# Optimization experiments

Hardware: AMD Instinct MI355X
Metric: run time of the kernel (lower is better)

## Reference

```python
import jax, jax.numpy as jnp
import numpy as np

B, N, K = 4, 8192, 10
_DIMS = [(12, 64), (64, 64), (128, 64), (64, 64), (128, 64), (192, 1024), (1216, 256), (256, 256), (256, 128), (128, 2)]


def setup_inputs() -> dict:
    key = jax.random.key(0)
    keys = jax.random.split(key, 12)
    inp = {"targets": jax.random.normal(keys[0], (B, N, 3), dtype=jnp.float32)}
    for i, (ci, co) in enumerate(_DIMS):
        a = float(np.sqrt(0.75 / ci))  # init_params: uniform(-sqrt(0.75/fan_in), +)
        inp[f"w{i + 1}"] = jax.random.uniform(keys[i + 1], (ci, co), minval=-a, maxval=a, dtype=jnp.float32)
    inp["prelu_a"] = 0.25 * jnp.ones((10,), jnp.float32)  # nn.PReLU default slope
    return inp


def _prelu(x, a):
    return jnp.where(x >= 0, x, a * x)


def _graph_features(x, k):
    # x: [N, C] -> edge features [N, k, 2C] (knn gather, diff, concat center)
    x2 = jnp.sum(x * x, axis=-1)
    d = x2[:, None] + x2[None, :] - 2.0 * (x @ x.T)  # [N, N] sq dists
    _, idx = jax.lax.top_k(-d, k)  # k nearest (includes self)
    nb = x[idx]  # [N, k, C]
    xr = jnp.broadcast_to(x[:, None, :], nb.shape)
    return jnp.concatenate([nb - xr, xr], axis=-1)


def _edge_conv(x, wa_list, k):
    # x: [B, N, C]; shared-MLP on edge features then max over k neighbors
    f = jax.vmap(lambda xb: _graph_features(xb, k))(x)  # [B, N, k, 2C]
    for w, a in wa_list:
        f = _prelu(f @ w, a)
    return jnp.max(f, axis=-2)  # [B, N, Cout]


def _forward(targets, ws, pa):
    # loss_f(targets) = 0.5*||targets||^2  =>  targets_grad = targets
    g = jax.grad(lambda t: 0.5 * jnp.sum(t * t))(targets)
    x = jnp.concatenate([targets, g], axis=-1)  # [B, N, 6]; hidden_features=0
    x1 = _edge_conv(x, [(ws[0], pa[0]), (ws[1], pa[1])], K)
    x2 = _edge_conv(x1, [(ws[2], pa[2]), (ws[3], pa[3])], K)
    x3 = _edge_conv(x2, [(ws[4], pa[4])], K)
    x4 = jnp.concatenate([x1, x2, x3], axis=-1)  # [B, N, 192]
    x5 = _prelu(x4 @ ws[5], pa[5])  # [B, N, 1024]
    x5 = jnp.broadcast_to(jnp.max(x5, axis=-2, keepdims=True), x5.shape)  # global max, repeated
    y = jnp.concatenate([x1, x2, x3, x5], axis=-1)  # [B, N, 1216]
    for i in range(6, 10):  # dropout is identity at eval
        y = _prelu(y @ ws[i], pa[i])
    return y[..., : 2]  # lr = y[..., :num_losses*2]; hidden slice is empty


def reference(targets, w1, w2, w3, w4, w5, w6, w7, w8, w9, w10, prelu_a):
    ws = [w1, w2, w3, w4, w5, w6, w7, w8, w9, w10]
    return _forward(targets, ws, prelu_a)
```

## Files before the change

kernel.cpp:

```cpp
#include <hip/hip_runtime.h>
#include <math.h>

#define NPTS 8192
#define KNNK 10

typedef __attribute__((ext_vector_type(8))) short bf16x8s;
typedef __attribute__((ext_vector_type(4))) float f32x4;

__device__ __forceinline__ float preluf(float v, float a){ return v >= 0.f ? v : a*v; }
__device__ __forceinline__ float4 f4fma(float a, float4 b, float4 c){
  return make_float4(fmaf(a,b.x,c.x), fmaf(a,b.y,c.y), fmaf(a,b.z,c.z), fmaf(a,b.w,c.w));
}

__device__ __forceinline__ void gl_lds16(const void* g, void* l){
  __builtin_amdgcn_global_load_lds((const __attribute__((address_space(1))) void*)g,
                                   (__attribute__((address_space(3))) void*)l, 16, 0, 0);
}
__device__ __forceinline__ void gl_lds4(const void* g, void* l){
  __builtin_amdgcn_global_load_lds((const __attribute__((address_space(1))) void*)g,
                                   (__attribute__((address_space(3))) void*)l, 4, 0, 0);
}

__device__ __forceinline__ void kinsd2(double* bk, float& g9, float pbd9, float d, int j){
  if (__any(d < g9)) {
    double t = (double)d;
    t = __longlong_as_double(__double_as_longlong(t) | (unsigned long long)(unsigned)j);
    #pragma unroll
    for (int s=0;s<10;++s){
      double mn = fmin(bk[s], t);
      double mx = fmax(bk[s], t);
      bk[s] = mn; t = mx;
    }
    g9 = fminf((float)bk[9], pbd9);
  }
}

__device__ __forceinline__ unsigned bfsplit2(float a, float b, unsigned& lo2){
  unsigned ua = __float_as_uint(a), ub = __float_as_uint(b);
  unsigned ha = (ua + 0x7FFFu + ((ua>>16)&1u)) & 0xFFFF0000u;
  unsigned hb = (ub + 0x7FFFu + ((ub>>16)&1u)) & 0xFFFF0000u;
  float ra = a - __uint_as_float(ha);
  float rb = b - __uint_as_float(hb);
  unsigned la = __float_as_uint(ra), lb = __float_as_uint(rb);
  unsigned qa = (la + 0x7FFFu + ((la>>16)&1u)) >> 16;
  unsigned qb = (lb + 0x7FFFu + ((lb>>16)&1u)) & 0xFFFF0000u;
  lo2 = qa | qb;
  return (ha >> 16) | hb;
}

__global__ __launch_bounds__(256) void prep0_kernel(const float* __restrict__ T,
                                                    float* __restrict__ x0,
                                                    float* __restrict__ sqn){
  int p = blockIdx.x*256 + threadIdx.x;
  float t0 = T[p*3+0], t1 = T[p*3+1], t2 = T[p*3+2];
  *(float4*)(x0 + (size_t)p*4) = make_float4(t0,t1,t2,0.f);
  float s = fmaf(t0,t0,0.f); s = fmaf(t1,t1,s); s = fmaf(t2,t2,s); s = fmaf(0.f,0.f,s);
  sqn[p] = s;
}

__global__ __launch_bounds__(256, 3) void knn64_kernel(const unsigned short* __restrict__ Xh,
                                                       const unsigned short* __restrict__ Xl,
                                                       const float* __restrict__ sqn,
                                                       double* __restrict__ pk){
  __shared__ __align__(16) unsigned char smem[52224];
  float* sx2j = (float*)(smem + 51200);
  double* lst = (double*)smem;

  const int b   = blockIdx.y;
  const int q0  = blockIdx.x * 128;
  const int jh  = blockIdx.z;
  const int NT  = (jh == 2) ? 22 : 21;
  const int jbase = jh * 2688;
  const int tid = threadIdx.x;
  const int L   = tid & 63;
  const int w   = tid >> 6;
  const int lm  = L & 15;
  const int kg  = L >> 4;
  const int rl  = L & 31;
  const int th  = L >> 5;

  float* dchw = (float*)(smem + 32768 + w*4608);

  const size_t bbase = (size_t)b * NPTS;

  bf16x8s ah[2][2], al[2][2];
  {
    const char* Ahp = (const char*)Xh + (bbase + q0 + w*32 + lm)*128;
    const char* Alp = (const char*)Xl + (bbase + q0 + w*32 + lm)*128;
    #pragma unroll
    for (int mt=0;mt<2;++mt)
      #pragma unroll
      for (int kc=0;kc<2;++kc){
        ah[mt][kc] = *(const bf16x8s*)(Ahp + mt*2048 + kc*64 + kg*16);
        al[mt][kc] = *(const bf16x8s*)(Alp + mt*2048 + kc*64 + kg*16);
      }
  }
  float x2qr[2][4];
  #pragma unroll
  for (int mt=0;mt<2;++mt)
    #pragma unroll
    for (int r=0;r<4;++r)
      x2qr[mt][r] = sqn[bbase + q0 + w*32 + mt*16 + kg*4 + r];

  const int srow = L >> 3;
  const unsigned soff = (unsigned)(((L & 7) ^ srow) << 4);
  const char* srch = (const char*)Xh + (bbase + (size_t)jbase + w*32 + srow)*128 + soff;
  const char* srcl = (const char*)Xl + (bbase + (size_t)jbase + w*32 + srow)*128 + soff;
  const float* sx2jsrc = sqn + bbase + jbase + w*64 + L;

  #pragma unroll
  for (int i=0;i<4;++i){
    gl_lds16(srch + i*1024, smem + w*4096 + i*1024);
    gl_lds16(srcl + i*1024, smem + 16384 + w*4096 + i*1024);
  }
  if (w < 2) gl_lds4(sx2jsrc, (char*)sx2j + w*256);

  double bk[10];
  float g9 = INFINITY, pbd9 = INFINITY;
  #pragma unroll
  for (int u=0;u<10;++u) bk[u] = (double)INFINITY;

  const char* xjh_c = (const char*)smem;
  const char* xjl_c = (const char*)smem + 16384;
  const unsigned swz = (unsigned)((lm & 7) << 4);

  for (int t = 0; t < NT; ++t) {
    __syncthreads();

    f32x4 acc[2][8];
    #pragma unroll
    for (int mt=0;mt<2;++mt)
      #pragma unroll
      for (int nt=0;nt<8;++nt) acc[mt][nt] = (f32x4){0.f,0.f,0.f,0.f};

    #pragma unroll
    for (int kc=0;kc<2;++kc){
      const unsigned koff = (unsigned)(kc*64 + kg*16) ^ swz;
      #pragma unroll
      for (int nt=0;nt<8;++nt){
        const int rb = (nt*16 + lm)*128;
        bf16x8s bh = *(const bf16x8s*)(xjh_c + rb + koff);
        bf16x8s bl = *(const bf16x8s*)(xjl_c + rb + koff);
        #pragma unroll
        for (int mt=0;mt<2;++mt){
          acc[mt][nt] = __builtin_amdgcn_mfma_f32_16x16x32_bf16(ah[mt][kc], bh, acc[mt][nt], 0,0,0);
          acc[mt][nt] = __builtin_amdgcn_mfma_f32_16x16x32_bf16(ah[mt][kc], bl, acc[mt][nt], 0,0,0);
          acc[mt][nt] = __builtin_amdgcn_mfma_f32_16x16x32_bf16(al[mt][kc], bh, acc[mt][nt], 0,0,0);
        }
      }
    }
    __syncthreads();

    if (t < NT-1){
      const char* nh = srch + (size_t)(t+1)*16384;
      const char* nl = srcl + (size_t)(t+1)*16384;
      #pragma unroll
      for (int i=0;i<4;++i){
        gl_lds16(nh + i*1024, smem + w*4096 + i*1024);
        gl_lds16(nl + i*1024, smem + 16384 + w*4096 + i*1024);
      }
      if (w < 2) gl_lds4(sx2jsrc + (size_t)(t+1)*128, (char*)sx2j + ((t+1)&1)*512 + w*256);
    }

    const int j0 = jbase + t*128;
    const float* x2jb = sx2j + (t&1)*128;

    #pragma unroll
    for (int cb=0; cb<4; ++cb){
      #pragma unroll
      for (int q2=0;q2<2;++q2){
        const int nt = cb*2 + q2;
        const int colc = q2*16 + lm;
        const float xj2 = x2jb[cb*32 + colc];
        #pragma unroll
        for (int mt=0;mt<2;++mt){
          f32x4 c = acc[mt][nt];
          #pragma unroll
          for (int r=0;r<4;++r)
            dchw[(mt*16 + kg*4 + r)*36 + colc] = x2qr[mt][r] + xj2 - 2.0f*c[r];
        }
      }
      asm volatile("" ::: "memory");
      const int jb0 = j0 + cb*32 + th*16;
      #pragma unroll
      for (int c4=0;c4<4;++c4){
        float4 dv = *(const float4*)&dchw[rl*36 + th*16 + c4*4];
        float m4 = fminf(fminf(dv.x,dv.y), fminf(dv.z,dv.w));
        if (__any(m4 < g9)){
          const int jj = jb0 + c4*4;
          kinsd2(bk, g9, pbd9, dv.x, jj);
          kinsd2(bk, g9, pbd9, dv.y, jj+1);
          kinsd2(bk, g9, pbd9, dv.z, jj+2);
          kinsd2(bk, g9, pbd9, dv.w, jj+3);
        }
      }
      asm volatile("" ::: "memory");
      float d9o = (float)bk[9];
      float p9  = __shfl_xor(d9o, 32);
      pbd9 = p9;
      g9 = fminf(d9o, p9);
    }
  }

  __syncthreads();
  #pragma unroll
  for (int u=0;u<10;++u) lst[(w*32 + rl)*20 + th*10 + u] = bk[u];
  __syncthreads();
  if (tid < 128) {
    const double* row = &lst[tid*20];
    int ia=0, ib=0;
    size_t base = ((size_t)jh*(4*NPTS) + bbase + q0 + tid)*10;
    #pragma unroll
    for (int u=0;u<10;++u){
      double ka = row[ia], kb2 = row[10+ib];
      bool ta = ka < kb2;
      pk[base+u] = ta ? ka : kb2;
      ia += ta ? 1 : 0; ib += ta ? 0 : 1;
    }
  }
}

__global__ __launch_bounds__(256, 2) void knn4_kernel(const float* __restrict__ X,
                                                      const float* __restrict__ sqn,
                                                      double* __restrict__ pk){
  __shared__ __align__(16) float xqT[4*132];
  __shared__ __align__(16) float uni[10752];
  __shared__ float s_x2q[128];
  __shared__ float s_x2j[128];
  __shared__ float sbd[2][128];

  const int b   = blockIdx.y;
  const int q0  = blockIdx.x * 128;
  const int jh  = blockIdx.z;
  const int tid = threadIdx.x;
  const int tn  = tid & 15;
  const int tm  = tid >> 4;
  const int tq  = tid & 127;
  const int th  = tid >> 7;

  const float* Xb = X + (size_t)b * NPTS * 4;

  for (int i = tid; i < 128; i += 256) {
    float4 v = *(const float4*)(Xb + (size_t)(q0+i)*4);
    xqT[0*132+i] = v.x; xqT[1*132+i] = v.y; xqT[2*132+i] = v.z; xqT[3*132+i] = v.w;
  }
  if (tid < 128) s_x2q[tid] = sqn[b*NPTS + q0 + tid];

  const int sw  = ((tn>>2)&3) << 2;
  const int bp0 = (tn*8)     ^ sw;
  const int bp1 = (tn*8 + 4) ^ sw;

  double bk[10];
  float g9 = INFINITY, pbd9 = INFINITY;
  #pragma unroll
  for (int u=0;u<10;++u) bk[u] = (double)INFINITY;

  for (int t = 0; t < 32; ++t) {
    const int j0 = jh*4096 + t*128;
    for (int i = tid; i < 128; i += 256) {
      float4 v = *(const float4*)(Xb + (size_t)(j0+i)*4);
      int pj = i ^ (((i>>5)&3) << 2);
      uni[0*132+pj] = v.x; uni[1*132+pj] = v.y; uni[2*132+pj] = v.z; uni[3*132+pj] = v.w;
    }
    if (tid < 128) s_x2j[tid] = sqn[b*NPTS + j0 + tid];
    __syncthreads();

    float acc[8][8];
    #pragma unroll
    for (int i=0;i<8;++i)
      #pragma unroll
      for (int j=0;j<8;++j) acc[i][j] = 0.f;

    #pragma unroll
    for (int kk=0; kk<4; ++kk) {
      float av[8], bv[8];
      *(float4*)&av[0] = *(const float4*)&xqT[kk*132 + tm*8];
      *(float4*)&av[4] = *(const float4*)&xqT[kk*132 + tm*8 + 4];
      *(float4*)&bv[0] = *(const float4*)&uni[kk*132 + bp0];
      *(float4*)&bv[4] = *(const float4*)&uni[kk*132 + bp1];
      #pragma unroll
      for (int i=0;i<8;++i)
        #pragma unroll
        for (int j=0;j<8;++j)
          acc[i][j] = fmaf(av[i], bv[j], acc[i][j]);
    }
    __syncthreads();

    #pragma unroll
    for (int h=0; h<2; ++h) {
      if ((tn>>3) == h) {
        #pragma unroll
        for (int qi=0; qi<8; ++qi) {
          const int row = tm*8 + qi;
          const float xq2 = s_x2q[row];
          float vv[8];
          #pragma unroll
          for (int u=0;u<8;++u)
            vv[u] = xq2 + s_x2j[tn*8 + u] - 2.f*acc[qi][u];
          *(float4*)&uni[row*68 + (tn&7)*8]     = make_float4(vv[0],vv[1],vv[2],vv[3]);
          *(float4*)&uni[row*68 + (tn&7)*8 + 4] = make_float4(vv[4],vv[5],vv[6],vv[7]);
        }
      }
      __syncthreads();
      {
        const int jb0 = j0 + h*64 + th*32;
        #pragma unroll
        for (int c4=0;c4<8;++c4){
          float4 dv = *(const float4*)&uni[tq*68 + th*32 + c4*4];
          int jj = jb0 + c4*4;
          kinsd2(bk, g9, pbd9, dv.x, jj);
          kinsd2(bk, g9, pbd9, dv.y, jj+1);
          kinsd2(bk, g9, pbd9, dv.z, jj+2);
          kinsd2(bk, g9, pbd9, dv.w, jj+3);
        }
      }
      if (h == 1) sbd[th][tq] = (float)bk[9];
      __syncthreads();
      if (h == 1){
        pbd9 = sbd[1^th][tq];
        g9 = fminf((float)bk[9], pbd9);
      }
    }
  }

  double* lst = (double*)uni;
  #pragma unroll
  for (int u=0;u<10;++u) lst[tq*20 + th*10 + u] = bk[u];
  __syncthreads();
  if (tid < 128) {
    const double* row = &lst[tid*20];
    int ia=0, ib=0;
    size_t base = ((size_t)jh*(4*NPTS) + (size_t)b*NPTS + q0 + tid)*10;
    #pragma unroll
    for (int u=0;u<10;++u){
      double ka = row[ia], kb2 = row[10+ib];
      bool ta = ka < kb2;
      pk[base+u] = ta ? ka : kb2;
      ia += ta ? 1 : 0; ib += ta ? 0 : 1;
    }
  }
}

__global__ __launch_bounds__(256) void knnmerge_kernel(const double* __restrict__ pk,
                                                       int* __restrict__ idxout){
  int p = blockIdx.x*256 + threadIdx.x;
  const double* A = pk + (size_t)p*10;
  const double* B = pk + (size_t)(4*NPTS)*10 + (size_t)p*10;
  int ia=0, ib=0;
  int* op = idxout + (size_t)p*10;
  #pragma unroll
  for (int u=0;u<10;++u){
    double ka = A[ia], kb = B[ib];
    bool t = ka < kb;
    op[u] = (int)(__double_as_longlong(t ? ka : kb) & 8191LL);
    ia += t ? 1 : 0; ib += t ? 0 : 1;
  }
}

__global__ __launch_bounds__(256) void knnmerge3_kernel(const double* __restrict__ pk,
                                                        int* __restrict__ idxout){
  int p = blockIdx.x*256 + threadIdx.x;
  const double* A = pk + (size_t)p*10;
  const double* B = pk + (size_t)(4*NPTS)*10 + (size_t)p*10;
  const double* C = pk + (size_t)(8*NPTS)*10 + (size_t)p*10;
  int ia=0, ib=0, ic=0;
  int* op = idxout + (size_t)p*10;
  #pragma unroll
  for (int u=0;u<10;++u){
    double ka = A[ia], kb = B[ib], kc = C[ic];
    bool tab = ka < kb; double mab = tab ? ka : kb;
    bool tc  = mab < kc; double m  = tc ? mab : kc;
    op[u] = (int)(__double_as_longlong(m) & 8191LL);
    ia += (tc && tab)  ? 1 : 0;
    ib += (tc && !tab) ? 1 : 0;
    ic += tc ? 0 : 1;
  }
}

__global__ __launch_bounds__(256) void prepUD64_kernel(const float* __restrict__ XC, int cin,
                                                       const float* __restrict__ W,
                                                       float* __restrict__ U,
                                                       float* __restrict__ D){
  const int tid = threadIdx.x;
  const int w = tid >> 6, o = tid & 63;
  const int p = blockIdx.x*4 + w;
  const float* xr = XC + (size_t)p*192 + cin;
  float zu = 0.f, zd = 0.f;
  #pragma unroll
  for (int c=0;c<64;++c){
    float xc = xr[c];
    float wt = W[c*64 + o];
    float wb = W[(64+c)*64 + o];
    zu = fmaf(xc, wt, zu);
    zd = fmaf(xc, wb - wt, zd);
  }
  U[(size_t)p*64 + o] = zu;
  D[(size_t)p*64 + o] = zd;
}

__global__ __launch_bounds__(256) void prepUD12_kernel(const float* __restrict__ T,
                                                       const float* __restrict__ W1,
                                                       float* __restrict__ U,
                                                       float* __restrict__ D){
  int p = blockIdx.x*256 + threadIdx.x;
  float t[3] = {T[p*3+0], T[p*3+1], T[p*3+2]};
  const float4* W = (const float4*)W1;
  float4 u[16], q[16];
  #pragma unroll
  for (int o=0;o<16;++o){ u[o]=make_float4(0,0,0,0); q[o]=make_float4(0,0,0,0); }
  #pragma unroll
  for (int c=0;c<3;++c){
    const float tc = t[c];
    #pragma unroll
    for (int o=0;o<16;++o){
      float4 ws  = W[c*16+o],     ws2 = W[(c+3)*16+o];
      float4 wq  = W[(c+6)*16+o], wq2 = W[(c+9)*16+o];
      u[o] = f4fma(tc, make_float4(ws.x+ws2.x, ws.y+ws2.y, ws.z+ws2.z, ws.w+ws2.w), u[o]);
      q[o] = f4fma(tc, make_float4(wq.x+wq2.x, wq.y+wq2.y, wq.z+wq2.z, wq.w+wq2.w), q[o]);
    }
  }
  float4* up = (float4*)(U + (size_t)p*64);
  float4* dp = (float4*)(D + (size_t)p*64);
  #pragma unroll
  for (int o=0;o<16;++o){
    up[o] = u[o];
    dp[o] = make_float4(q[o].x-u[o].x, q[o].y-u[o].y, q[o].z-u[o].z, q[o].w-u[o].w);
  }
}

__global__ __launch_bounds__(256) void edge2w_kernel(const float* __restrict__ U,
                                                     const float* __restrict__ Dp,
                                                     const int* __restrict__ idx,
                                                     const float* __restrict__ Wb,
                                                     const float* __restrict__ PA, int paa, int pab,
                                                     float* __restrict__ out, int coff,
                                                     float* __restrict__ sqnout,
                                                     unsigned short* __restrict__ Xh,
                                                     unsigned short* __restrict__ Xl){
  __shared__ __align__(16) float sh[4][10][68];
  const int tid = threadIdx.x;
  const int w = tid >> 6, o = tid & 63;
  const int p = blockIdx.x*4 + w, b = p >> 13;
  const float aa = PA[paa], ab = PA[pab];

  float wreg[64];
  #pragma unroll
  for (int c=0;c<64;++c) wreg[c] = Wb[c*64 + o];

  const float dc = Dp[(size_t)p*64 + o];

  #pragma unroll
  for (int k=0;k<10;++k){
    int nb = idx[p*10 + k];
    float u = U[((size_t)(b<<13)+nb)*64 + o];
    sh[w][k][o] = preluf(u + dc, aa);
  }
  __syncthreads();

  float mx = -INFINITY;
  #pragma unroll 2
  for (int k=0;k<10;++k){
    float a0=0.f,a1=0.f,a2=0.f,a3=0.f;
    #pragma unroll
    for (int c4=0;c4<16;++c4){
      float4 hv = *(const float4*)&sh[w][k][c4*4];
      a0 = fmaf(hv.x, wreg[c4*4+0], a0);
      a1 = fmaf(hv.y, wreg[c4*4+1], a1);
      a2 = fmaf(hv.z, wreg[c4*4+2], a2);
      a3 = fmaf(hv.w, wreg[c4*4+3], a3);
    }
    float z = (a0+a1)+(a2+a3);
    mx = fmaxf(mx, preluf(z, ab));
  }
  out[(size_t)p*192 + coff + o] = mx;
  {
    unsigned um = __float_as_uint(mx);
    unsigned h  = (um + 0x7FFFu + ((um>>16)&1u)) & 0xFFFF0000u;
    float rr = mx - __uint_as_float(h);
    unsigned ur = __float_as_uint(rr);
    unsigned l  = (ur + 0x7FFFu + ((ur>>16)&1u)) >> 16;
    Xh[(size_t)p*64 + o] = (unsigned short)(h >> 16);
    Xl[(size_t)p*64 + o] = (unsigned short)l;
  }
  float sq = mx*mx;
  #pragma unroll
  for (int off=1; off<64; off<<=1) sq += __shfl_xor(sq, off);
  if (o == 0) sqnout[p] = sq;
}

__global__ __launch_bounds__(256) void edge1w_kernel(const float* __restrict__ U,
                                                     const float* __restrict__ Dp,
                                                     const int* __restrict__ idx,
                                                     const float* __restrict__ PA, int paa,
                                                     float* __restrict__ out, int coff){
  const int tid = threadIdx.x;
  const int w = tid >> 6, o = tid & 63;
  const int p = blockIdx.x*4 + w, b = p >> 13;
  const float aa = PA[paa];
  const float dc = Dp[(size_t)p*64 + o];
  float mx = -INFINITY;
  #pragma unroll
  for (int k=0;k<10;++k){
    int nb = idx[p*10 + k];
    float u = U[((size_t)(b<<13)+nb)*64 + o];
    mx = fmaxf(mx, preluf(u + dc, aa));
  }
  out[(size_t)p*192 + coff + o] = mx;
}

__global__ __launch_bounds__(256) void prepWall_kernel(const float* __restrict__ W6,
                                                       const float* __restrict__ W7,
                                                       const float* __restrict__ W8,
                                                       const float* __restrict__ W9,
                                                       unsigned short* __restrict__ Wh6, unsigned short* __restrict__ Wl6,
                                                       unsigned short* __restrict__ Wh7, unsigned short* __restrict__ Wl7,
                                                       unsigned short* __restrict__ Wh8, unsigned short* __restrict__ Wl8,
                                                       unsigned short* __restrict__ Wh9, unsigned short* __restrict__ Wl9){
  int bb = blockIdx.x;
  const float* W; unsigned short *Wh, *Wl; int K, N, k;
  if (bb < 192)      { W=W6; Wh=Wh6; Wl=Wl6; K=192; N=1024; k=bb; }
  else if (bb < 384) { W=W7; Wh=Wh7; Wl=Wl7; K=192; N=256;  k=bb-192; }
  else if (bb < 640) { W=W8; Wh=Wh8; Wl=Wl8; K=256; N=256;  k=bb-384; }
  else               { W=W9; Wh=Wh9; Wl=Wl9; K=256; N=128;  k=bb-640; }
  for (int n = threadIdx.x; n < N; n += 256){
    float v = W[(size_t)k*N + n];
    unsigned ua = __float_as_uint(v);
    unsigned h = (ua + 0x7FFFu + ((ua>>16)&1u)) & 0xFFFF0000u;
    float r = v - __uint_as_float(h);
    unsigned ub = __float_as_uint(r);
    unsigned l = (ub + 0x7FFFu + ((ub>>16)&1u)) >> 16;
    Wh[(size_t)n*K + k] = (unsigned short)(h >> 16);
    Wl[(size_t)n*K + k] = (unsigned short)l;
  }
}

template<int EPI>
__global__ __launch_bounds__(256, 2) void mgemm_kernel(const float* __restrict__ A, int lda,
                                                       const unsigned short* __restrict__ WhT,
                                                       const unsigned short* __restrict__ WlT,
                                                       int K,
                                                       float* __restrict__ C, int ldc,
                                                       const float* __restrict__ bias,
                                                       const float* __restrict__ PA, int pidx,
                                                       int Ntot){
  __shared__ __align__(16) unsigned char smem[73728];
  unsigned short* sa = (unsigned short*)smem;
  unsigned short* sb = (unsigned short*)(smem + 36864);
  float* cst = (float*)smem;

  const int tid = threadIdx.x;
  const int m0 = blockIdx.x*128, n0 = blockIdx.y*128;
  const int L = tid & 63, w = tid >> 6;
  const int lm = L & 15, kg = L >> 4;

  f32x4 acc[2][8];
  #pragma unroll
  for (int mt=0;mt<2;++mt)
    #pragma unroll
    for (int nt=0;nt<8;++nt) acc[mt][nt] = (f32x4){0.f,0.f,0.f,0.f};

  for (int c0 = 0; c0 < K; c0 += 64) {
    __syncthreads();
    #pragma unroll
    for (int s=0;s<8;++s){
      int e = tid + s*256;
      int r = e >> 4, kq = (e & 15) << 2;
      float4 v = *(const float4*)(A + (size_t)(m0+r)*lda + c0 + kq);
      unsigned lo01, lo23;
      unsigned hi01 = bfsplit2(v.x, v.y, lo01);
      unsigned hi23 = bfsplit2(v.z, v.w, lo23);
      uint2 hp; hp.x = hi01; hp.y = hi23;
      uint2 lp; lp.x = lo01; lp.y = lo23;
      *(uint2*)&sa[r*72 + kq]        = hp;
      *(uint2*)&sa[9216 + r*72 + kq] = lp;
    }
    #pragma unroll
    for (int s=0;s<4;++s){
      int e = tid + s*256;
      int col = e >> 3, ko = (e & 7) << 3;
      *(uint4*)&sb[col*72 + ko]        = *(const uint4*)&WhT[(size_t)(n0+col)*K + c0 + ko];
      *(uint4*)&sb[9216 + col*72 + ko] = *(const uint4*)&WlT[(size_t)(n0+col)*K + c0 + ko];
    }
    __syncthreads();

    #pragma unroll
    for (int kc=0;kc<2;++kc){
      const int ko = kc*32 + kg*8;
      bf16x8s ah[2], al[2];
      #pragma unroll
      for (int mt=0;mt<2;++mt){
        int q = w*32 + mt*16 + lm;
        ah[mt] = *(const bf16x8s*)&sa[q*72 + ko];
        al[mt] = *(const bf16x8s*)&sa[9216 + q*72 + ko];
      }
      #pragma unroll
      for (int nt=0;nt<8;++nt){
        int n = nt*16 + lm;
        bf16x8s bh = *(const bf16x8s*)&sb[n*72 + ko];
        bf16x8s bl = *(const bf16x8s*)&sb[9216 + n*72 + ko];
        #pragma unroll
        for (int mt=0;mt<2;++mt){
          acc[mt][nt] = __builtin_amdgcn_mfma_f32_16x16x32_bf16(ah[mt], bh, acc[mt][nt], 0,0,0);
          acc[mt][nt] = __builtin_amdgcn_mfma_f32_16x16x32_bf16(ah[mt], bl, acc[mt][nt], 0,0,0);
          acc[mt][nt] = __builtin_amdgcn_mfma_f32_16x16x32_bf16(al[mt], bh, acc[mt][nt], 0,0,0);
        }
      }
    }
  }
  __syncthreads();

  const float a = PA[pidx];
  if (EPI == 2) {
    #pragma unroll
    for (int nt=0;nt<8;++nt){
      f32x4 c0v = acc[0][nt], c1v = acc[1][nt];
      float m = -INFINITY;
      #pragma unroll
      for (int r=0;r<4;++r){ m = fmaxf(m, preluf(c0v[r], a)); m = fmaxf(m, preluf(c1v[r], a)); }
      m = fmaxf(m, __shfl_xor(m, 16));
      m = fmaxf(m, __shfl_xor(m, 32));
      if (kg == 0) cst[w*128 + nt*16 + lm] = m;
    }
    __syncthreads();
    if (tid < 128){
      float m = fmaxf(fmaxf(cst[tid], cst[128+tid]), fmaxf(cst[256+tid], cst[384+tid]));
      C[(size_t)blockIdx.x*Ntot + n0 + tid] = m;
    }
  } else {
    float bc[8];
    if (EPI == 1){
      int bb = m0 >> 13;
      #pragma unroll
      for (int nt=0;nt<8;++nt) bc[nt] = bias[bb*256 + n0 + nt*16 + lm];
    }
    #pragma unroll
    for (int mt=0;mt<2;++mt){
      #pragma unroll
      for (int nt=0;nt<8;++nt){
        f32x4 c = acc[mt][nt];
        int col = nt*16 + lm;
        #pragma unroll
        for (int r=0;r<4;++r){
          int row = w*32 + mt*16 + kg*4 + r;
          float v = c[r] + (EPI==1 ? bc[nt] : 0.f);
          cst[row*132 + col] = preluf(v, a);
        }
      }
    }
    __syncthreads();
    const int tm = tid & 15, tn = tid >> 4;
    #pragma unroll
    for (int i=0;i<8;++i){
      int row = tm*8 + i;
      float4 v0 = *(const float4*)&cst[row*132 + tn*8];
      float4 v1 = *(const float4*)&cst[row*132 + tn*8 + 4];
      float* cp = C + (size_t)(m0 + row)*ldc + n0 + tn*8;
      *(float4*)cp     = v0;
      *(float4*)(cp+4) = v1;
    }
  }
}

__global__ __launch_bounds__(256) void reduce_pmax(const float* __restrict__ pmax,
                                                   float* __restrict__ x5m){
  int t = blockIdx.x*256 + threadIdx.x;
  if (t < 4096) {
    int b = t >> 10, o = t & 1023;
    float m = -INFINITY;
    for (int mt=0; mt<64; ++mt) m = fmaxf(m, pmax[((size_t)(b*64+mt))*1024 + o]);
    x5m[t] = m;
  }
}

__global__ __launch_bounds__(256) void bias7_kernel(const float* __restrict__ x5m,
                                                    const float* __restrict__ W7,
                                                    float* __restrict__ b7){
  int b = blockIdx.x; int o = threadIdx.x;
  float s = 0.f;
  for (int j=0;j<1024;++j) s = fmaf(x5m[b*1024+j], W7[(size_t)(192+j)*256 + o], s);
  b7[b*256+o] = s;
}

__global__ __launch_bounds__(256) void final10_kernel(const float* __restrict__ y3,
                                                      const float* __restrict__ W10,
                                                      const float* __restrict__ PA,
                                                      float* __restrict__ out){
  int p = blockIdx.x*256 + threadIdx.x;
  const float4* r = (const float4*)(y3 + (size_t)p*128);
  float s0=0.f, s1=0.f;
  #pragma unroll
  for (int c4=0;c4<32;++c4){
    float4 v = r[c4];
    s0 = fmaf(v.x, W10[(c4*4+0)*2+0], s0); s1 = fmaf(v.x, W10[(c4*4+0)*2+1], s1);
    s0 = fmaf(v.y, W10[(c4*4+1)*2+0], s0); s1 = fmaf(v.y, W10[(c4*4+1)*2+1], s1);
    s0 = fmaf(v.z, W10[(c4*4+2)*2+0], s0); s1 = fmaf(v.z, W10[(c4*4+2)*2+1], s1);
    s0 = fmaf(v.w, W10[(c4*4+3)*2+0], s0); s1 = fmaf(v.w, W10[(c4*4+3)*2+1], s1);
  }
  float a = PA[9];
  out[p*2+0] = s0>=0.f? s0 : a*s0;
  out[p*2+1] = s1>=0.f? s1 : a*s1;
}

extern "C" void kernel_launch(void* const* d_in, const int* in_sizes, int n_in,
                              void* d_out, int out_size, void* d_ws, size_t ws_size,
                              hipStream_t stream) {
  const float* T   = (const float*)d_in[0];
  const float* W1  = (const float*)d_in[1];
  const float* W2  = (const float*)d_in[2];
  const float* W3  = (const float*)d_in[3];
  const float* W4  = (const float*)d_in[4];
  const float* W5  = (const float*)d_in[5];
  const float* W6  = (const float*)d_in[6];
  const float* W7  = (const float*)d_in[7];
  const float* W8  = (const float*)d_in[8];
  const float* W9  = (const float*)d_in[9];
  const float* W10 = (const float*)d_in[10];
  const float* PA  = (const float*)d_in[11];

  float* ws   = (float*)d_ws;
  float* x0   = ws + 0;
  float* sqn0 = ws + 131072;
  float* sqn1 = ws + 163840;
  float* sqn2 = ws + 196608;
  int*   idx0 = (int*)(ws + 229376);
  int*   idx1 = (int*)(ws + 557056);
  int*   idx2 = (int*)(ws + 884736);
  float* xcat = ws + 1212416;
  float* pmax = ws + 7503872;
  float* x5m  = ws + 7766016;
  float* b7   = ws + 7770112;
  float* y1   = ws + 7771136;
  float* y2   = ws + 16159744;
  float* y3   = xcat;
  float* U    = y1;
  float* D    = y2;
  double* pk  = (double*)y1;
  unsigned short* Xh = (unsigned short*)(y1 + 3145728);
  unsigned short* Xl = (unsigned short*)(y1 + 4194304);

  unsigned short* wsc = (unsigned short*)(ws + 229376);
  unsigned short* Wh6 = wsc;
  unsigned short* Wl6 = wsc + 196608;
  unsigned short* Wh7 = wsc + 393216;
  unsigned short* Wl7 = wsc + 442368;
  unsigned short* Wh8 = wsc + 491520;
  unsigned short* Wl8 = wsc + 557056;
  unsigned short* Wh9 = wsc + 622592;
  unsigned short* Wl9 = wsc + 655360;

  prep0_kernel<<<128, 256, 0, stream>>>(T, x0, sqn0);
  knn4_kernel<<<dim3(64,4,2), 256, 0, stream>>>(x0, sqn0, pk);
  knnmerge_kernel<<<128, 256, 0, stream>>>(pk, idx0);
  prepUD12_kernel<<<128, 256, 0, stream>>>(T, W1, U, D);
  edge2w_kernel<<<8192, 256, 0, stream>>>(U, D, idx0, W2, PA, 0, 1, xcat, 0, sqn1, Xh, Xl);

  knn64_kernel<<<dim3(64,4,3), 256, 0, stream>>>(Xh, Xl, sqn1, pk);
  knnmerge3_kernel<<<128, 256, 0, stream>>>(pk, idx1);
  prepUD64_kernel<<<8192, 256, 0, stream>>>(xcat, 0, W3, U, D);
  edge2w_kernel<<<8192, 256, 0, stream>>>(U, D, idx1, W4, PA, 2, 3, xcat, 64, sqn2, Xh, Xl);

  knn64_kernel<<<dim3(64,4,3), 256, 0, stream>>>(Xh, Xl, sqn2, pk);
  knnmerge3_kernel<<<128, 256, 0, stream>>>(pk, idx2);
  prepUD64_kernel<<<8192, 256, 0, stream>>>(xcat, 64, W5, U, D);
  edge1w_kernel<<<8192, 256, 0, stream>>>(U, D, idx2, PA, 4, xcat, 128);

  prepWall_kernel<<<896, 256, 0, stream>>>(W6, W7, W8, W9,
                                           Wh6, Wl6, Wh7, Wl7, Wh8, Wl8, Wh9, Wl9);

  mgemm_kernel<2><<<dim3(256,8), 256, 0, stream>>>(xcat, 192, Wh6, Wl6, 192, pmax, 0, nullptr, PA, 5, 1024);
  reduce_pmax<<<16, 256, 0, stream>>>(pmax, x5m);
  bias7_kernel<<<4, 256, 0, stream>>>(x5m, W7, b7);
  mgemm_kernel<1><<<dim3(256,2), 256, 0, stream>>>(xcat, 192, Wh7, Wl7, 192, y1, 256, b7, PA, 6, 0);
  mgemm_kernel<0><<<dim3(256,2), 256, 0, stream>>>(y1, 256, Wh8, Wl8, 256, y2, 256, nullptr, PA, 7, 0);
  mgemm_kernel<0><<<dim3(256,1), 256, 0, stream>>>(y2, 256, Wh9, Wl9, 256, y3, 128, nullptr, PA, 8, 0);
  final10_kernel<<<128, 256, 0, stream>>>(y3, W10, PA, (float*)d_out);
}
```

Baseline: 1.509 ms.

## Restructure knn64 to swap MFMA operands and select top-k from registers

The 64-dim kNN kernel now takes 64 queries per block instead of 128. It swaps the MFMA operands so each lane directly holds four candidate distances for its own query. This removes the LDS staging of the distance tile and its readback. The candidate range is split into two halves of 4096 instead of three segments, so the cheaper two-way merge kernel replaces the three-way one. In exchange, each block keeps four partial top-k lists per query that are merged in shared memory, the threshold now needs cross-lane shuffles over 4 lane groups, and less query data is reused per loaded candidate tile.

```diff
diff --git a/kernel.cpp b/kernel.cpp
--- a/kernel.cpp
+++ b/kernel.cpp
@@ -58,55 +58,43 @@
   sqn[p] = s;
 }
 
-__global__ __launch_bounds__(256, 3) void knn64_kernel(const unsigned short* __restrict__ Xh,
+__global__ __launch_bounds__(256, 4) void knn64_kernel(const unsigned short* __restrict__ Xh,
                                                        const unsigned short* __restrict__ Xl,
                                                        const float* __restrict__ sqn,
                                                        double* __restrict__ pk){
-  __shared__ __align__(16) unsigned char smem[52224];
-  float* sx2j = (float*)(smem + 51200);
+  __shared__ __align__(16) unsigned char smem[33792];
+  float* sx2j = (float*)(smem + 32768);
   double* lst = (double*)smem;
 
   const int b   = blockIdx.y;
-  const int q0  = blockIdx.x * 128;
+  const int q0  = blockIdx.x * 64;
   const int jh  = blockIdx.z;
-  const int NT  = (jh == 2) ? 22 : 21;
-  const int jbase = jh * 2688;
   const int tid = threadIdx.x;
   const int L   = tid & 63;
   const int w   = tid >> 6;
   const int lm  = L & 15;
   const int kg  = L >> 4;
-  const int rl  = L & 31;
-  const int th  = L >> 5;
-
-  float* dchw = (float*)(smem + 32768 + w*4608);
 
   const size_t bbase = (size_t)b * NPTS;
-
-  bf16x8s ah[2][2], al[2][2];
+  const int qi = q0 + w*16 + lm;
+
+  bf16x8s qh[2], ql[2];
   {
-    const char* Ahp = (const char*)Xh + (bbase + q0 + w*32 + lm)*128;
-    const char* Alp = (const char*)Xl + (bbase + q0 + w*32 + lm)*128;
-    #pragma unroll
-    for (int mt=0;mt<2;++mt)
-      #pragma unroll
-      for (int kc=0;kc<2;++kc){
-        ah[mt][kc] = *(const bf16x8s*)(Ahp + mt*2048 + kc*64 + kg*16);
-        al[mt][kc] = *(const bf16x8s*)(Alp + mt*2048 + kc*64 + kg*16);
-      }
-  }
-  float x2qr[2][4];
-  #pragma unroll
-  for (int mt=0;mt<2;++mt)
-    #pragma unroll
-    for (int r=0;r<4;++r)
-      x2qr[mt][r] = sqn[bbase + q0 + w*32 + mt*16 + kg*4 + r];
+    const char* Qh = (const char*)Xh + (bbase + qi)*128;
+    const char* Ql = (const char*)Xl + (bbase + qi)*128;
+    #pragma unroll
+    for (int kc=0;kc<2;++kc){
+      qh[kc] = *(const bf16x8s*)(Qh + kc*64 + kg*16);
+      ql[kc] = *(const bf16x8s*)(Ql + kc*64 + kg*16);
+    }
+  }
+  const float x2q = sqn[bbase + qi];
 
   const int srow = L >> 3;
   const unsigned soff = (unsigned)(((L & 7) ^ srow) << 4);
-  const char* srch = (const char*)Xh + (bbase + (size_t)jbase + w*32 + srow)*128 + soff;
-  const char* srcl = (const char*)Xl + (bbase + (size_t)jbase + w*32 + srow)*128 + soff;
-  const float* sx2jsrc = sqn + bbase + jbase + w*64 + L;
+  const char* srch = (const char*)Xh + (bbase + (size_t)jh*4096 + w*32 + srow)*128 + soff;
+  const char* srcl = (const char*)Xl + (bbase + (size_t)jh*4096 + w*32 + srow)*128 + soff;
+  const float* sx2jsrc = sqn + bbase + jh*4096 + w*64 + L;
 
   #pragma unroll
   for (int i=0;i<4;++i){
@@ -124,34 +112,29 @@
   const char* xjl_c = (const char*)smem + 16384;
   const unsigned swz = (unsigned)((lm & 7) << 4);
 
-  for (int t = 0; t < NT; ++t) {
+  for (int t = 0; t < 32; ++t) {
     __syncthreads();
 
-    f32x4 acc[2][8];
-    #pragma unroll
-    for (int mt=0;mt<2;++mt)
-      #pragma unroll
-      for (int nt=0;nt<8;++nt) acc[mt][nt] = (f32x4){0.f,0.f,0.f,0.f};
+    f32x4 acc[8];
+    #pragma unroll
+    for (int jb=0;jb<8;++jb) acc[jb] = (f32x4){0.f,0.f,0.f,0.f};
 
     #pragma unroll
     for (int kc=0;kc<2;++kc){
       const unsigned koff = (unsigned)(kc*64 + kg*16) ^ swz;
       #pragma unroll
-      for (int nt=0;nt<8;++nt){
-        const int rb = (nt*16 + lm)*128;
-        bf16x8s bh = *(const bf16x8s*)(xjh_c + rb + koff);
-        bf16x8s bl = *(const bf16x8s*)(xjl_c + rb + koff);
-        #pragma unroll
-        for (int mt=0;mt<2;++mt){
-          acc[mt][nt] = __builtin_amdgcn_mfma_f32_16x16x32_bf16(ah[mt][kc], bh, acc[mt][nt], 0,0,0);
-          acc[mt][nt] = __builtin_amdgcn_mfma_f32_16x16x32_bf16(ah[mt][kc], bl, acc[mt][nt], 0,0,0);
-          acc[mt][nt] = __builtin_amdgcn_mfma_f32_16x16x32_bf16(al[mt][kc], bh, acc[mt][nt], 0,0,0);
-        }
+      for (int jb=0;jb<8;++jb){
+        const int rb = (jb*16 + lm)*128;
+        bf16x8s jhf = *(const bf16x8s*)(xjh_c + rb + koff);
+        bf16x8s jlf = *(const bf16x8s*)(xjl_c + rb + koff);
+        acc[jb] = __builtin_amdgcn_mfma_f32_16x16x32_bf16(jhf, qh[kc], acc[jb], 0,0,0);
+        acc[jb] = __builtin_amdgcn_mfma_f32_16x16x32_bf16(jlf, qh[kc], acc[jb], 0,0,0);
+        acc[jb] = __builtin_amdgcn_mfma_f32_16x16x32_bf16(jhf, ql[kc], acc[jb], 0,0,0);
       }
     }
     __syncthreads();
 
-    if (t < NT-1){
+    if (t < 31){
       const char* nh = srch + (size_t)(t+1)*16384;
       const char* nl = srcl + (size_t)(t+1)*16384;
       #pragma unroll
@@ -162,60 +145,54 @@
       if (w < 2) gl_lds4(sx2jsrc + (size_t)(t+1)*128, (char*)sx2j + ((t+1)&1)*512 + w*256);
     }
 
-    const int j0 = jbase + t*128;
+    const int j0 = jh*4096 + t*128;
     const float* x2jb = sx2j + (t&1)*128;
 
     #pragma unroll
-    for (int cb=0; cb<4; ++cb){
-      #pragma unroll
-      for (int q2=0;q2<2;++q2){
-        const int nt = cb*2 + q2;
-        const int colc = q2*16 + lm;
-        const float xj2 = x2jb[cb*32 + colc];
-        #pragma unroll
-        for (int mt=0;mt<2;++mt){
-          f32x4 c = acc[mt][nt];
-          #pragma unroll
-          for (int r=0;r<4;++r)
-            dchw[(mt*16 + kg*4 + r)*36 + colc] = x2qr[mt][r] + xj2 - 2.0f*c[r];
-        }
-      }
-      asm volatile("" ::: "memory");
-      const int jb0 = j0 + cb*32 + th*16;
-      #pragma unroll
-      for (int c4=0;c4<4;++c4){
-        float4 dv = *(const float4*)&dchw[rl*36 + th*16 + c4*4];
-        float m4 = fminf(fminf(dv.x,dv.y), fminf(dv.z,dv.w));
-        if (__any(m4 < g9)){
-          const int jj = jb0 + c4*4;
-          kinsd2(bk, g9, pbd9, dv.x, jj);
-          kinsd2(bk, g9, pbd9, dv.y, jj+1);
-          kinsd2(bk, g9, pbd9, dv.z, jj+2);
-          kinsd2(bk, g9, pbd9, dv.w, jj+3);
-        }
-      }
-      asm volatile("" ::: "memory");
-      float d9o = (float)bk[9];
-      float p9  = __shfl_xor(d9o, 32);
-      pbd9 = p9;
-      g9 = fminf(d9o, p9);
+    for (int jb=0;jb<8;++jb){
+      float4 xj2 = *(const float4*)&x2jb[jb*16 + kg*4];
+      f32x4 c = acc[jb];
+      float4 dv = make_float4(x2q + xj2.x - 2.0f*c[0],
+                              x2q + xj2.y - 2.0f*c[1],
+                              x2q + xj2.z - 2.0f*c[2],
+                              x2q + xj2.w - 2.0f*c[3]);
+      float m4 = fminf(fminf(dv.x,dv.y), fminf(dv.z,dv.w));
+      if (__any(m4 < g9)){
+        const int jj = j0 + jb*16 + kg*4;
+        kinsd2(bk, g9, pbd9, dv.x, jj);
+        kinsd2(bk, g9, pbd9, dv.y, jj+1);
+        kinsd2(bk, g9, pbd9, dv.z, jj+2);
+        kinsd2(bk, g9, pbd9, dv.w, jj+3);
+      }
+      if (jb & 1){
+        float d9 = (float)bk[9];
+        float m  = fminf(d9, __shfl_xor(d9, 16));
+        float mm = fminf(m,  __shfl_xor(m, 32));
+        pbd9 = mm;
+        g9 = mm;
+      }
     }
   }
 
   __syncthreads();
   #pragma unroll
-  for (int u=0;u<10;++u) lst[(w*32 + rl)*20 + th*10 + u] = bk[u];
+  for (int u=0;u<10;++u) lst[(size_t)(w*16 + lm)*40 + kg*10 + u] = bk[u];
   __syncthreads();
-  if (tid < 128) {
-    const double* row = &lst[tid*20];
-    int ia=0, ib=0;
+  if (tid < 64) {
+    const double* row = &lst[(size_t)tid*40];
+    int i0=0, i1=0, i2=0, i3=0;
     size_t base = ((size_t)jh*(4*NPTS) + bbase + q0 + tid)*10;
     #pragma unroll
     for (int u=0;u<10;++u){
-      double ka = row[ia], kb2 = row[10+ib];
-      bool ta = ka < kb2;
-      pk[base+u] = ta ? ka : kb2;
-      ia += ta ? 1 : 0; ib += ta ? 0 : 1;
+      double ka = row[i0], kb2 = row[10+i1], kc2 = row[20+i2], kd2 = row[30+i3];
+      bool tab = ka  < kb2; double mab = tab ? ka  : kb2;
+      bool tcd = kc2 < kd2; double mcd = tcd ? kc2 : kd2;
+      bool tt  = mab < mcd; double m   = tt  ? mab : mcd;
+      pk[base+u] = m;
+      i0 += (tt && tab)  ? 1 : 0;
+      i1 += (tt && !tab) ? 1 : 0;
+      i2 += (!tt && tcd) ? 1 : 0;
+      i3 += (!tt && !tcd)? 1 : 0;
     }
   }
 }
@@ -354,26 +331,6 @@
     bool t = ka < kb;
     op[u] = (int)(__double_as_longlong(t ? ka : kb) & 8191LL);
     ia += t ? 1 : 0; ib += t ? 0 : 1;
-  }
-}
-
-__global__ __launch_bounds__(256) void knnmerge3_kernel(const double* __restrict__ pk,
-                                                        int* __restrict__ idxout){
-  int p = blockIdx.x*256 + threadIdx.x;
-  const double* A = pk + (size_t)p*10;
-  const double* B = pk + (size_t)(4*NPTS)*10 + (size_t)p*10;
-  const double* C = pk + (size_t)(8*NPTS)*10 + (size_t)p*10;
-  int ia=0, ib=0, ic=0;
-  int* op = idxout + (size_t)p*10;
-  #pragma unroll
-  for (int u=0;u<10;++u){
-    double ka = A[ia], kb = B[ib], kc = C[ic];
-    bool tab = ka < kb; double mab = tab ? ka : kb;
-    bool tc  = mab < kc; double m  = tc ? mab : kc;
-    op[u] = (int)(__double_as_longlong(m) & 8191LL);
-    ia += (tc && tab)  ? 1 : 0;
-    ib += (tc && !tab) ? 1 : 0;
-    ic += tc ? 0 : 1;
   }
 }
 
@@ -754,13 +711,13 @@
   prepUD12_kernel<<<128, 256, 0, stream>>>(T, W1, U, D);
   edge2w_kernel<<<8192, 256, 0, stream>>>(U, D, idx0, W2, PA, 0, 1, xcat, 0, sqn1, Xh, Xl);
 
-  knn64_kernel<<<dim3(64,4,3), 256, 0, stream>>>(Xh, Xl, sqn1, pk);
-  knnmerge3_kernel<<<128, 256, 0, stream>>>(pk, idx1);
+  knn64_kernel<<<dim3(128,4,2), 256, 0, stream>>>(Xh, Xl, sqn1, pk);
+  knnmerge_kernel<<<128, 256, 0, stream>>>(pk, idx1);
   prepUD64_kernel<<<8192, 256, 0, stream>>>(xcat, 0, W3, U, D);
   edge2w_kernel<<<8192, 256, 0, stream>>>(U, D, idx1, W4, PA, 2, 3, xcat, 64, sqn2, Xh, Xl);
 
-  knn64_kernel<<<dim3(64,4,3), 256, 0, stream>>>(Xh, Xl, sqn2, pk);
-  knnmerge3_kernel<<<128, 256, 0, stream>>>(pk, idx2);
+  knn64_kernel<<<dim3(128,4,2), 256, 0, stream>>>(Xh, Xl, sqn2, pk);
+  knnmerge_kernel<<<128, 256, 0, stream>>>(pk, idx2);
   prepUD64_kernel<<<8192, 256, 0, stream>>>(xcat, 64, W5, U, D);
   edge1w_kernel<<<8192, 256, 0, stream>>>(U, D, idx2, PA, 4, xcat, 128);
 
```

After: 1.523 ms. Within noise of the previous version (+0.9%).
